# Kernel tuning notes

Measured on AMD Instinct MI355X. Metric: run time of the kernel, lower is better.

Reference implementation:

```python
import jax, jax.numpy as jnp
import numpy as np

NH, NKV, D = 16, 8, 128
HID = 2048
EPS = 1e-6
ROPE_BASE = 10000.0
T = 2048


def setup_inputs() -> dict:
    key = jax.random.key(0)
    k1, k2, k3 = jax.random.split(key, 3)
    return {
        "positions": jnp.arange(T, dtype=jnp.int32),
        "hidden_states": jax.random.normal(k1, (T, HID), dtype=jnp.float32),
        "w_qkv": jax.random.normal(k2, (HID, (NH + 2 * NKV) * D), dtype=jnp.float32) * 0.02,
        "w_o": jax.random.normal(k3, (NH * D, HID), dtype=jnp.float32) * 0.02,
        "q_norm_w": jnp.ones((D,), dtype=jnp.float32),
        "k_norm_w": jnp.ones((D,), dtype=jnp.float32),
    }


def _rmsnorm(x, w):
    # per-head RMSNorm over last dim (head_dim)
    return x * jax.lax.rsqrt(jnp.mean(x * x, axis=-1, keepdims=True) + EPS) * w


def reference(positions, hidden_states, w_qkv, w_o, q_norm_w, k_norm_w):
    t = hidden_states.shape[0]
    scale = D ** -0.5

    # fused QKV projection, then split
    qkv = hidden_states @ w_qkv                       # [T, (NH+2*NKV)*D]
    q, k, v = jnp.split(qkv, [NH * D, (NH + NKV) * D], axis=-1)
    q = q.reshape(t, NH, D)
    k = k.reshape(t, NKV, D)
    v = v.reshape(t, NKV, D)

    # per-head QK RMSNorm (Qwen3)
    q = _rmsnorm(q, q_norm_w)
    k = _rmsnorm(k, k_norm_w)

    # RoPE (neox style: rotate half-split pairs)
    inv_freq = 1.0 / (ROPE_BASE ** (jnp.arange(0, D, 2, dtype=jnp.float32) / D))
    freqs = positions.astype(jnp.float32)[:, None] * inv_freq  # [T, D/2]
    cos = jnp.cos(freqs)[:, None, :]                   # [T, 1, D/2]
    sin = jnp.sin(freqs)[:, None, :]

    def rope(x):
        x1, x2 = jnp.split(x, 2, axis=-1)
        return jnp.concatenate([x1 * cos - x2 * sin, x2 * cos + x1 * sin], axis=-1)

    q = rope(q)
    k = rope(k)

    # GQA: repeat kv heads
    g = NH // NKV
    kr = jnp.repeat(k, g, axis=1)                      # [T, NH, D]
    vr = jnp.repeat(v, g, axis=1)

    # causal attention
    scores = jnp.einsum('thd,shd->hts', q, kr) * scale  # [NH, T, T]
    causal = jnp.tril(jnp.ones((t, t), dtype=bool))
    scores = jnp.where(causal[None], scores, -jnp.inf)
    probs = jax.nn.softmax(scores, axis=-1)
    o = jnp.einsum('hts,shd->thd', probs, vr).reshape(t, NH * D)

    return o @ w_o
```

## Files before the change

### kernel.cpp

```cpp
#include <hip/hip_runtime.h>
#include <math.h>

#define T_TOK 2048
#define HIDDEN 2048
#define NH 16
#define NKV 8
#define DH 128

typedef unsigned short u16;
typedef __attribute__((ext_vector_type(8))) short bf16x8;
typedef __attribute__((ext_vector_type(4))) float f32x4;

__device__ __forceinline__ u16 f2bf(float f) {
  union { float f; unsigned u; } x; x.f = f;
  unsigned r = (x.u + 0x7fffu + ((x.u >> 16) & 1u)) >> 16;
  return (u16)r;
}

__device__ __forceinline__ float bf2f(u16 v) {
  union { unsigned u; float f; } x; x.u = ((unsigned)v) << 16;
  return x.f;
}

__device__ __forceinline__ void gload16(const void* g, void* l) {
  __builtin_amdgcn_global_load_lds((const __attribute__((address_space(1))) void*)g,
                                   (__attribute__((address_space(3))) void*)l,
                                   16, 0, 0);
}

__global__ __launch_bounds__(256) void prepass(const float* __restrict__ hidden,
                                               const float* __restrict__ w_qkv,
                                               const float* __restrict__ w_o,
                                               u16* __restrict__ Xb,
                                               u16* __restrict__ WqkvT,
                                               u16* __restrict__ WoT) {
  __shared__ float tile[64][65];
  const int b = blockIdx.x;
  if (b < 4096) {
    int i = b * 256 + threadIdx.x;
    float4 v = ((const float4*)hidden)[i];
    ushort4 o;
    o.x = f2bf(v.x); o.y = f2bf(v.y); o.z = f2bf(v.z); o.w = f2bf(v.w);
    ((ushort4*)Xb)[i] = o;
    return;
  }
  const float* in; u16* out; int R, Cdim, c0, r0;
  if (b < 6144) {
    int bb = b - 4096;
    in = w_qkv; out = WqkvT; R = 2048; Cdim = 4096;
    c0 = (bb & 63) * 64; r0 = (bb >> 6) * 64;
  } else {
    int bb = b - 6144;
    in = w_o; out = WoT; R = 2048; Cdim = 2048;
    c0 = (bb & 31) * 64; r0 = (bb >> 5) * 64;
  }
  const int tx = threadIdx.x & 63, ty = threadIdx.x >> 6;
#pragma unroll
  for (int i = 0; i < 64; i += 4)
    tile[ty + i][tx] = in[(size_t)(r0 + ty + i) * Cdim + c0 + tx];
  __syncthreads();
#pragma unroll
  for (int i = 0; i < 64; i += 4)
    out[(size_t)(c0 + ty + i) * R + r0 + tx] = f2bf(tile[tx][ty + i]);
}

__global__ __launch_bounds__(256) void add_parts4(const u16* __restrict__ a,
                                                  const u16* __restrict__ b,
                                                  const u16* __restrict__ c,
                                                  const u16* __restrict__ d,
                                                  float* __restrict__ o, int n4) {
  int i = blockIdx.x * blockDim.x + threadIdx.x;
  if (i < n4) {
    ushort4 x = ((const ushort4*)a)[i], y = ((const ushort4*)b)[i];
    ushort4 u = ((const ushort4*)c)[i], v = ((const ushort4*)d)[i];
    float4 z;
    z.x = bf2f(x.x) + bf2f(y.x) + bf2f(u.x) + bf2f(v.x);
    z.y = bf2f(x.y) + bf2f(y.y) + bf2f(u.y) + bf2f(v.y);
    z.z = bf2f(x.z) + bf2f(y.z) + bf2f(u.z) + bf2f(v.z);
    z.w = bf2f(x.w) + bf2f(y.w) + bf2f(u.w) + bf2f(v.w);
    ((float4*)o)[i] = z;
  }
}

__global__ __launch_bounds__(256) void rope_vt(const u16* __restrict__ qkv0,
                                               const u16* __restrict__ qkv1,
                                               const int* __restrict__ pos,
                                               const float* __restrict__ qw,
                                               const float* __restrict__ kw,
                                               u16* __restrict__ Qg,
                                               u16* __restrict__ Kg,
                                               u16* __restrict__ Vt,
                                               unsigned* __restrict__ counter) {
  __shared__ float tile[64][65];
  const int b = blockIdx.x;
  if (b < 12288) {
    const int wave = threadIdx.x >> 6, j = threadIdx.x & 63;
    const int idx = b * 4 + wave;
    const int t = idx & 2047, slot = idx >> 11;
    const float QSC = 0.088388347648318447f * 1.4426950408889634f;
    const size_t base_i = (size_t)t * 4096 + slot * 128;
    float x1 = bf2f(qkv0[base_i + j]) + bf2f(qkv1[base_i + j]);
    float x2 = bf2f(qkv0[base_i + j + 64]) + bf2f(qkv1[base_i + j + 64]);
    float ss = x1 * x1 + x2 * x2;
#pragma unroll
    for (int m = 1; m < 64; m <<= 1) ss += __shfl_xor(ss, m);
    float r = rsqrtf(ss * (1.0f / 128.0f) + 1e-6f);
    const bool isq = slot < NH;
    const float* w = isq ? qw : kw;
    float xn1 = x1 * r * w[j], xn2 = x2 * r * w[j + 64];
    float fp = (float)pos[t];
    float inv_freq = exp2f(-(float)j * (13.287712379549449f / 64.0f));
    float ang = fp * inv_freq;
    float sn, cs;
    sincosf(ang, &sn, &cs);
    float o1 = xn1 * cs - xn2 * sn;
    float o2 = xn2 * cs + xn1 * sn;
    if (isq) {
      size_t base = ((size_t)slot * T_TOK + t) * DH;
      Qg[base + j] = f2bf(o1 * QSC); Qg[base + 64 + j] = f2bf(o2 * QSC);
    } else {
      size_t base = ((size_t)(slot - NH) * T_TOK + t) * DH;
      Kg[base + j] = f2bf(o1); Kg[base + 64 + j] = f2bf(o2);
    }
    return;
  }
  if (b == 12288 && threadIdx.x == 0) *counter = 0u;
  const int bb = b - 12288;
  const int h = bb & 7, rest = bb >> 3;
  const int t0 = (rest & 31) * 64, d0 = (rest >> 5) * 64;
  const int tx = threadIdx.x & 63, ty = threadIdx.x >> 6;
#pragma unroll
  for (int i = 0; i < 64; i += 4) {
    size_t gi = (size_t)(t0 + ty + i) * 4096 + (NH + NKV) * DH + h * DH + d0 + tx;
    tile[ty + i][tx] = bf2f(qkv0[gi]) + bf2f(qkv1[gi]);
  }
  __syncthreads();
#pragma unroll
  for (int i = 0; i < 64; i += 4)
    Vt[((size_t)h * DH + d0 + ty + i) * T_TOK + t0 + tx] = f2bf(tile[tx][ty + i]);
}

__global__ __launch_bounds__(256) void gemm_bf16(const u16* __restrict__ A,
                                                 const u16* __restrict__ Bt,
                                                 void* __restrict__ Cout,
                                                 int M, int N, int K, int lda, int ldb,
                                                 int obf16) {
  __shared__ u16 Alds[128 * 64];
  __shared__ u16 Blds[128 * 64];
  A += (size_t)blockIdx.z * K;
  Bt += (size_t)blockIdx.z * K;
  const int m0 = blockIdx.y * 128, n0 = blockIdx.x * 128;
  const int wave = threadIdx.x >> 6, lane = threadIdx.x & 63;
  const int l15 = lane & 15, quad = lane >> 4;
  const int wr = wave >> 1, wc = wave & 1;

  const f32x4 zero = {0.f, 0.f, 0.f, 0.f};
  f32x4 acc[4][4];
#pragma unroll
  for (int i = 0; i < 4; ++i)
#pragma unroll
    for (int j = 0; j < 4; ++j) acc[i][j] = zero;

  for (int k0 = 0; k0 < K; k0 += 64) {
    __syncthreads();
#pragma unroll
    for (int c = 0; c < 4; ++c) {
      int chunk = wave * 4 + c;
      int slot = chunk * 64 + lane;
      int row = slot >> 3;
      int g = (slot & 7) ^ (row & 7);
      gload16(A + (size_t)(m0 + row) * lda + k0 + g * 8, &Alds[chunk * 512]);
      gload16(Bt + (size_t)(n0 + row) * ldb + k0 + g * 8, &Blds[chunk * 512]);
    }
    __syncthreads();
#pragma unroll
    for (int ksub = 0; ksub < 2; ++ksub) {
      bf16x8 af[4], bfr[4];
#pragma unroll
      for (int mt = 0; mt < 4; ++mt) {
        int r = wr * 64 + mt * 16 + l15;
        af[mt] = *(const bf16x8*)&Alds[r * 64 + (((ksub * 4 + quad) ^ (r & 7)) * 8)];
      }
#pragma unroll
      for (int nt = 0; nt < 4; ++nt) {
        int r = wc * 64 + nt * 16 + l15;
        bfr[nt] = *(const bf16x8*)&Blds[r * 64 + (((ksub * 4 + quad) ^ (r & 7)) * 8)];
      }
#pragma unroll
      for (int mt = 0; mt < 4; ++mt)
#pragma unroll
        for (int nt = 0; nt < 4; ++nt)
          acc[mt][nt] = __builtin_amdgcn_mfma_f32_16x16x32_bf16(af[mt], bfr[nt], acc[mt][nt], 0, 0, 0);
    }
  }
  if (obf16) {
    u16* C = (u16*)Cout + (size_t)blockIdx.z * M * N;
#pragma unroll
    for (int mt = 0; mt < 4; ++mt)
#pragma unroll
      for (int nt = 0; nt < 4; ++nt)
#pragma unroll
        for (int r = 0; r < 4; ++r)
          C[(size_t)(m0 + wr * 64 + mt * 16 + quad * 4 + r) * N + n0 + wc * 64 + nt * 16 + l15] =
              f2bf(acc[mt][nt][r]);
  } else {
    float* C = (float*)Cout + (size_t)blockIdx.z * M * N;
#pragma unroll
    for (int mt = 0; mt < 4; ++mt)
#pragma unroll
      for (int nt = 0; nt < 4; ++nt)
#pragma unroll
        for (int r = 0; r < 4; ++r)
          C[(size_t)(m0 + wr * 64 + mt * 16 + quad * 4 + r) * N + n0 + wc * 64 + nt * 16 + l15] =
              acc[mt][nt][r];
  }
}

__global__ __launch_bounds__(256) void attn_kernel(const u16* __restrict__ Qg,
                                                   const u16* __restrict__ Kg,
                                                   const u16* __restrict__ Vtg,
                                                   float* __restrict__ Opart,
                                                   float* __restrict__ Lpart,
                                                   unsigned* __restrict__ counter) {
  __shared__ u16 Klds[64 * 128];
  __shared__ u16 Vlds[128 * 64];
  __shared__ u16 Plds[4][16 * 72];
  __shared__ unsigned item_s;
  const int wave = threadIdx.x >> 6, lane = threadIdx.x & 63;
  const int l15 = lane & 15, quad = lane >> 4;
  u16* Pw = &Plds[wave][0];
  const f32x4 zero = {0.f, 0.f, 0.f, 0.f};
  const float4 zero4 = {0.f, 0.f, 0.f, 0.f};

  for (;;) {
    __syncthreads();
    if (threadIdx.x == 0) item_s = atomicAdd(counter, 1u);
    __syncthreads();
    const unsigned item = item_s;
    if (item >= 1024u) break;
    const int qt = 31 - (int)(item >> 5);
    const int s  = (int)(item >> 4) & 1;
    const int h  = (int)item & 15;
    const int kvh = h >> 1;
    const int slot = (h * 32 + qt) * 2 + s;
    const int j0 = s ? (qt + 2) >> 1 : 0;
    const int j1 = s ? qt + 1 : (qt + 2) >> 1;

    float* Oslot = Opart + (size_t)slot * (64 * 128);

    if (j0 >= j1) {
      for (int t = threadIdx.x; t < 64 * 128 / 4; t += 256) ((float4*)Oslot)[t] = zero4;
      if (threadIdx.x < 64) Lpart[slot * 64 + threadIdx.x] = 0.f;
      continue;
    }

    const u16* Qh = Qg + (size_t)h * T_TOK * DH;
    const u16* Kh = Kg + (size_t)kvh * T_TOK * DH;
    const u16* Vh = Vtg + (size_t)kvh * DH * T_TOK;
    const int qrow0 = qt * 64 + wave * 16;

    bf16x8 qf[4];
#pragma unroll
    for (int ks = 0; ks < 4; ++ks)
      qf[ks] = *(const bf16x8*)(Qh + (size_t)(qrow0 + l15) * DH + ks * 32 + quad * 8);

    f32x4 oacc[8];
#pragma unroll
    for (int i = 0; i < 8; ++i) oacc[i] = zero;
    float l_i[4] = {0.f, 0.f, 0.f, 0.f};

    for (int j = j0; j < j1; ++j) {
      __syncthreads();
#pragma unroll
      for (int c = 0; c < 4; ++c) {
        int chunk = wave * 4 + c;
        int sl = chunk * 64 + lane;
        {
          int ss = sl >> 4;
          int g = (sl & 15) ^ (ss & 15);
          gload16(Kh + ((size_t)(j * 64 + ss)) * DH + g * 8, &Klds[chunk * 512]);
        }
        {
          int d = sl >> 3;
          int g = (sl & 7) ^ (d & 7);
          gload16(Vh + (size_t)d * T_TOK + j * 64 + g * 8, &Vlds[chunk * 512]);
        }
      }
      __syncthreads();

      f32x4 sacc[4];
#pragma unroll
      for (int nt = 0; nt < 4; ++nt) sacc[nt] = zero;
#pragma unroll
      for (int nt = 0; nt < 4; ++nt) {
        int sr = nt * 16 + l15;
#pragma unroll
        for (int ks = 0; ks < 4; ++ks) {
          bf16x8 kf = *(const bf16x8*)&Klds[sr * 128 + (((ks * 4 + quad) ^ (sr & 15)) * 8)];
          sacc[nt] = __builtin_amdgcn_mfma_f32_16x16x32_bf16(qf[ks], kf, sacc[nt], 0, 0, 0);
        }
      }

      if (j == qt) {
#pragma unroll
        for (int nt = 0; nt < 4; ++nt)
#pragma unroll
          for (int r = 0; r < 4; ++r) {
            int col = j * 64 + nt * 16 + l15;
            int row = qrow0 + quad * 4 + r;
            if (col > row) sacc[nt][r] = -INFINITY;
          }
      }

#pragma unroll
      for (int nt = 0; nt < 4; ++nt)
#pragma unroll
        for (int r = 0; r < 4; ++r) {
          float pv = exp2f(sacc[nt][r]);
          unsigned u = __float_as_uint(pv);
          Pw[(quad * 4 + r) * 72 + nt * 16 + l15] = (u16)(u >> 16);
          l_i[r] += __uint_as_float(u & 0xffff0000u);
        }

      bf16x8 pf[2];
#pragma unroll
      for (int ks = 0; ks < 2; ++ks)
        pf[ks] = *(const bf16x8*)&Pw[l15 * 72 + ks * 32 + quad * 8];
#pragma unroll
      for (int ot = 0; ot < 8; ++ot) {
        int d = ot * 16 + l15;
#pragma unroll
        for (int ks = 0; ks < 2; ++ks) {
          bf16x8 vf = *(const bf16x8*)&Vlds[d * 64 + (((ks * 4 + quad) ^ (d & 7)) * 8)];
          oacc[ot] = __builtin_amdgcn_mfma_f32_16x16x32_bf16(pf[ks], vf, oacc[ot], 0, 0, 0);
        }
      }
    }

#pragma unroll
    for (int ot = 0; ot < 8; ++ot)
#pragma unroll
      for (int r = 0; r < 4; ++r)
        Oslot[(wave * 16 + quad * 4 + r) * 128 + ot * 16 + l15] = oacc[ot][r];
#pragma unroll
    for (int msk = 1; msk < 16; msk <<= 1)
#pragma unroll
      for (int r = 0; r < 4; ++r) l_i[r] += __shfl_xor(l_i[r], msk);
    if (l15 == 0) {
#pragma unroll
      for (int r = 0; r < 4; ++r)
        Lpart[slot * 64 + wave * 16 + quad * 4 + r] = l_i[r];
    }
  }
}

__global__ __launch_bounds__(256) void attn_merge(const float* __restrict__ Opart,
                                                  const float* __restrict__ Lpart,
                                                  u16* __restrict__ Og) {
  const int b = blockIdx.x;
  const int h = b & 15, qt = b >> 4;
  const int slot0 = (h * 32 + qt) * 2, slot1 = slot0 + 1;
  const float4* O0 = (const float4*)(Opart + (size_t)slot0 * (64 * 128));
  const float4* O1 = (const float4*)(Opart + (size_t)slot1 * (64 * 128));
#pragma unroll
  for (int it = 0; it < 8; ++it) {
    int idx = it * 256 + threadIdx.x;
    int r = idx >> 5, c4 = idx & 31;
    float rl = 1.0f / (Lpart[slot0 * 64 + r] + Lpart[slot1 * 64 + r]);
    float4 a = O0[idx], c = O1[idx];
    int row = qt * 64 + r, col = c4 * 4;
    u16* dst = Og + (size_t)row * (NH * DH) + h * DH + col;
    dst[0] = f2bf((a.x + c.x) * rl);
    dst[1] = f2bf((a.y + c.y) * rl);
    dst[2] = f2bf((a.z + c.z) * rl);
    dst[3] = f2bf((a.w + c.w) * rl);
  }
}

extern "C" void kernel_launch(void* const* d_in, const int* in_sizes, int n_in,
                              void* d_out, int out_size, void* d_ws, size_t ws_size,
                              hipStream_t stream) {
  (void)in_sizes; (void)n_in; (void)out_size; (void)ws_size;
  const int* positions = (const int*)d_in[0];
  const float* hidden  = (const float*)d_in[1];
  const float* w_qkv   = (const float*)d_in[2];
  const float* w_o     = (const float*)d_in[3];
  const float* q_norm  = (const float*)d_in[4];
  const float* k_norm  = (const float*)d_in[5];
  float* out = (float*)d_out;

  char* ws = (char*)d_ws;
  u16*   Xb    = (u16*)(ws);
  u16*   WqkvT = (u16*)(ws + ( 8ull << 20));
  u16*   WoT   = (u16*)(ws + (24ull << 20));
  u16*   P0    = (u16*)(ws + (32ull << 20));
  u16*   P1    = P0 + (size_t)T_TOK * 4096;
  u16*   Qg    = (u16*)(ws + (64ull << 20));
  u16*   Kg    = (u16*)(ws + (72ull << 20));
  u16*   Vt    = (u16*)(ws + (76ull << 20));
  u16*   AttnO = (u16*)(ws + (80ull << 20));
  float* Opart = (float*)(ws + (32ull << 20));
  float* Lpart = (float*)(ws);
  unsigned* ctr = (unsigned*)(ws + (512ull << 10));
  u16*   G2P   = (u16*)(ws + (32ull << 20));

  prepass<<<dim3(7168), 256, 0, stream>>>(hidden, w_qkv, w_o, Xb, WqkvT, WoT);

  gemm_bf16<<<dim3(4096 / 128, T_TOK / 128, 2), 256, 0, stream>>>(
      Xb, WqkvT, P0, T_TOK, 4096, 1024, HIDDEN, HIDDEN, 1);

  rope_vt<<<dim3(12288 + 512), 256, 0, stream>>>(P0, P1, positions,
                                                 q_norm, k_norm, Qg, Kg, Vt, ctr);

  attn_kernel<<<dim3(768), 256, 0, stream>>>(Qg, Kg, Vt, Opart, Lpart, ctr);
  attn_merge<<<dim3(512), 256, 0, stream>>>(Opart, Lpart, AttnO);

  gemm_bf16<<<dim3(HIDDEN / 128, T_TOK / 128, 4), 256, 0, stream>>>(
      AttnO, WoT, G2P, T_TOK, HIDDEN, 512, NH * DH, NH * DH, 1);
  const int n4 = T_TOK * HIDDEN / 4;
  add_parts4<<<dim3(n4 / 256), 256, 0, stream>>>(
      G2P, G2P + (size_t)T_TOK * HIDDEN, G2P + 2 * (size_t)T_TOK * HIDDEN,
      G2P + 3 * (size_t)T_TOK * HIDDEN, out, n4);
}
```

Measured before the change: 259.7 us.

## Fuse attention merge into attention kernel via completion flags; reduce split-K parts

Removes the separate attn_merge launch. The attention kernel now writes normalized bf16 output directly when a tile needs no split. For split tiles, the second finishing block (detected via a per-tile atomic flag after a threadfence) performs the merge. Empty split halves are now skipped instead of writing zeros. Also adds an XOR-swizzled P layout in LDS in place of the padded stride, raises the attention grid and occupancy hint, and halves the output projection's split-K factor so the final add reads two partial buffers instead of four. In exchange it depends on correct fence and flag ordering across blocks, and the output GEMM has fewer blocks to run in parallel.

```diff
diff --git a/kernel.cpp b/kernel.cpp
--- a/kernel.cpp
+++ b/kernel.cpp
@@ -64,20 +64,17 @@
     out[(size_t)(c0 + ty + i) * R + r0 + tx] = f2bf(tile[tx][ty + i]);
 }
 
-__global__ __launch_bounds__(256) void add_parts4(const u16* __restrict__ a,
+__global__ __launch_bounds__(256) void add_parts2(const u16* __restrict__ a,
                                                   const u16* __restrict__ b,
-                                                  const u16* __restrict__ c,
-                                                  const u16* __restrict__ d,
                                                   float* __restrict__ o, int n4) {
   int i = blockIdx.x * blockDim.x + threadIdx.x;
   if (i < n4) {
     ushort4 x = ((const ushort4*)a)[i], y = ((const ushort4*)b)[i];
-    ushort4 u = ((const ushort4*)c)[i], v = ((const ushort4*)d)[i];
     float4 z;
-    z.x = bf2f(x.x) + bf2f(y.x) + bf2f(u.x) + bf2f(v.x);
-    z.y = bf2f(x.y) + bf2f(y.y) + bf2f(u.y) + bf2f(v.y);
-    z.z = bf2f(x.z) + bf2f(y.z) + bf2f(u.z) + bf2f(v.z);
-    z.w = bf2f(x.w) + bf2f(y.w) + bf2f(u.w) + bf2f(v.w);
+    z.x = bf2f(x.x) + bf2f(y.x);
+    z.y = bf2f(x.y) + bf2f(y.y);
+    z.z = bf2f(x.z) + bf2f(y.z);
+    z.w = bf2f(x.w) + bf2f(y.w);
     ((float4*)o)[i] = z;
   }
 }
@@ -90,7 +87,8 @@
                                                u16* __restrict__ Qg,
                                                u16* __restrict__ Kg,
                                                u16* __restrict__ Vt,
-                                               unsigned* __restrict__ counter) {
+                                               unsigned* __restrict__ counter,
+                                               unsigned* __restrict__ flags) {
   __shared__ float tile[64][65];
   const int b = blockIdx.x;
   if (b < 12288) {
@@ -124,7 +122,11 @@
     }
     return;
   }
-  if (b == 12288 && threadIdx.x == 0) *counter = 0u;
+  if (b == 12288) {
+    if (threadIdx.x == 0) *counter = 0u;
+    flags[threadIdx.x] = 0u;
+    flags[threadIdx.x + 256] = 0u;
+  }
   const int bb = b - 12288;
   const int h = bb & 7, rest = bb >> 3;
   const int t0 = (rest & 31) * 64, d0 = (rest >> 5) * 64;
@@ -216,27 +218,28 @@
   }
 }
 
-__global__ __launch_bounds__(256) void attn_kernel(const u16* __restrict__ Qg,
-                                                   const u16* __restrict__ Kg,
-                                                   const u16* __restrict__ Vtg,
-                                                   float* __restrict__ Opart,
-                                                   float* __restrict__ Lpart,
-                                                   unsigned* __restrict__ counter) {
+__global__ __launch_bounds__(256, 4) void attn_kernel(const u16* __restrict__ Qg,
+                                                      const u16* __restrict__ Kg,
+                                                      const u16* __restrict__ Vtg,
+                                                      float* __restrict__ Opart,
+                                                      float* __restrict__ Lpart,
+                                                      unsigned* __restrict__ counter,
+                                                      unsigned* __restrict__ flags,
+                                                      u16* __restrict__ Og) {
   __shared__ u16 Klds[64 * 128];
   __shared__ u16 Vlds[128 * 64];
-  __shared__ u16 Plds[4][16 * 72];
-  __shared__ unsigned item_s;
+  __shared__ u16 Plds[4][16 * 64];
+  unsigned* shq = (unsigned*)&Plds[0][0];
   const int wave = threadIdx.x >> 6, lane = threadIdx.x & 63;
   const int l15 = lane & 15, quad = lane >> 4;
   u16* Pw = &Plds[wave][0];
   const f32x4 zero = {0.f, 0.f, 0.f, 0.f};
-  const float4 zero4 = {0.f, 0.f, 0.f, 0.f};
 
   for (;;) {
     __syncthreads();
-    if (threadIdx.x == 0) item_s = atomicAdd(counter, 1u);
-    __syncthreads();
-    const unsigned item = item_s;
+    if (threadIdx.x == 0) shq[0] = atomicAdd(counter, 1u);
+    __syncthreads();
+    const unsigned item = shq[0];
     if (item >= 1024u) break;
     const int qt = 31 - (int)(item >> 5);
     const int s  = (int)(item >> 4) & 1;
@@ -245,14 +248,7 @@
     const int slot = (h * 32 + qt) * 2 + s;
     const int j0 = s ? (qt + 2) >> 1 : 0;
     const int j1 = s ? qt + 1 : (qt + 2) >> 1;
-
-    float* Oslot = Opart + (size_t)slot * (64 * 128);
-
-    if (j0 >= j1) {
-      for (int t = threadIdx.x; t < 64 * 128 / 4; t += 256) ((float4*)Oslot)[t] = zero4;
-      if (threadIdx.x < 64) Lpart[slot * 64 + threadIdx.x] = 0.f;
-      continue;
-    }
+    if (j0 >= j1) continue;
 
     const u16* Qh = Qg + (size_t)h * T_TOK * DH;
     const u16* Kh = Kg + (size_t)kvh * T_TOK * DH;
@@ -318,14 +314,16 @@
         for (int r = 0; r < 4; ++r) {
           float pv = exp2f(sacc[nt][r]);
           unsigned u = __float_as_uint(pv);
-          Pw[(quad * 4 + r) * 72 + nt * 16 + l15] = (u16)(u >> 16);
+          int row = quad * 4 + r;
+          int c = nt * 16 + l15;
+          Pw[row * 64 + (((c >> 3) ^ (row & 7)) * 8) + (c & 7)] = (u16)(u >> 16);
           l_i[r] += __uint_as_float(u & 0xffff0000u);
         }
 
       bf16x8 pf[2];
 #pragma unroll
       for (int ks = 0; ks < 2; ++ks)
-        pf[ks] = *(const bf16x8*)&Pw[l15 * 72 + ks * 32 + quad * 8];
+        pf[ks] = *(const bf16x8*)&Pw[l15 * 64 + (((ks * 4 + quad) ^ (l15 & 7)) * 8)];
 #pragma unroll
       for (int ot = 0; ot < 8; ++ot) {
         int d = ot * 16 + l15;
@@ -338,42 +336,58 @@
     }
 
 #pragma unroll
+    for (int msk = 1; msk < 16; msk <<= 1)
+#pragma unroll
+      for (int r = 0; r < 4; ++r) l_i[r] += __shfl_xor(l_i[r], msk);
+
+    if (j0 == 0 && j1 == qt + 1) {
+      float rl[4];
+#pragma unroll
+      for (int r = 0; r < 4; ++r) rl[r] = 1.0f / l_i[r];
+#pragma unroll
+      for (int ot = 0; ot < 8; ++ot)
+#pragma unroll
+        for (int r = 0; r < 4; ++r) {
+          int row = qrow0 + quad * 4 + r;
+          Og[(size_t)row * (NH * DH) + h * DH + ot * 16 + l15] = f2bf(oacc[ot][r] * rl[r]);
+        }
+      continue;
+    }
+
+    float* Oslot = Opart + (size_t)slot * (64 * 128);
+#pragma unroll
     for (int ot = 0; ot < 8; ++ot)
 #pragma unroll
       for (int r = 0; r < 4; ++r)
         Oslot[(wave * 16 + quad * 4 + r) * 128 + ot * 16 + l15] = oacc[ot][r];
-#pragma unroll
-    for (int msk = 1; msk < 16; msk <<= 1)
-#pragma unroll
-      for (int r = 0; r < 4; ++r) l_i[r] += __shfl_xor(l_i[r], msk);
     if (l15 == 0) {
 #pragma unroll
       for (int r = 0; r < 4; ++r)
         Lpart[slot * 64 + wave * 16 + quad * 4 + r] = l_i[r];
     }
-  }
-}
-
-__global__ __launch_bounds__(256) void attn_merge(const float* __restrict__ Opart,
-                                                  const float* __restrict__ Lpart,
-                                                  u16* __restrict__ Og) {
-  const int b = blockIdx.x;
-  const int h = b & 15, qt = b >> 4;
-  const int slot0 = (h * 32 + qt) * 2, slot1 = slot0 + 1;
-  const float4* O0 = (const float4*)(Opart + (size_t)slot0 * (64 * 128));
-  const float4* O1 = (const float4*)(Opart + (size_t)slot1 * (64 * 128));
-#pragma unroll
-  for (int it = 0; it < 8; ++it) {
-    int idx = it * 256 + threadIdx.x;
-    int r = idx >> 5, c4 = idx & 31;
-    float rl = 1.0f / (Lpart[slot0 * 64 + r] + Lpart[slot1 * 64 + r]);
-    float4 a = O0[idx], c = O1[idx];
-    int row = qt * 64 + r, col = c4 * 4;
-    u16* dst = Og + (size_t)row * (NH * DH) + h * DH + col;
-    dst[0] = f2bf((a.x + c.x) * rl);
-    dst[1] = f2bf((a.y + c.y) * rl);
-    dst[2] = f2bf((a.z + c.z) * rl);
-    dst[3] = f2bf((a.w + c.w) * rl);
+    __threadfence();
+    __syncthreads();
+    if (threadIdx.x == 0) shq[1] = atomicAdd(&flags[h * 32 + qt], 1u);
+    __syncthreads();
+    if (shq[1] == 1u) {
+      __threadfence();
+      const int slot0 = (h * 32 + qt) * 2, slot1 = slot0 + 1;
+      const float4* O0 = (const float4*)(Opart + (size_t)slot0 * (64 * 128));
+      const float4* O1 = (const float4*)(Opart + (size_t)slot1 * (64 * 128));
+#pragma unroll
+      for (int it = 0; it < 8; ++it) {
+        int idx = it * 256 + threadIdx.x;
+        int r = idx >> 5, c4 = idx & 31;
+        float rl = 1.0f / (Lpart[slot0 * 64 + r] + Lpart[slot1 * 64 + r]);
+        float4 a = O0[idx], c = O1[idx];
+        int row = qt * 64 + r, col = c4 * 4;
+        u16* dst = Og + (size_t)row * (NH * DH) + h * DH + col;
+        dst[0] = f2bf((a.x + c.x) * rl);
+        dst[1] = f2bf((a.y + c.y) * rl);
+        dst[2] = f2bf((a.z + c.z) * rl);
+        dst[3] = f2bf((a.w + c.w) * rl);
+      }
+    }
   }
 }
 
@@ -401,7 +415,8 @@
   u16*   AttnO = (u16*)(ws + (80ull << 20));
   float* Opart = (float*)(ws + (32ull << 20));
   float* Lpart = (float*)(ws);
-  unsigned* ctr = (unsigned*)(ws + (512ull << 10));
+  unsigned* ctr   = (unsigned*)(ws + (512ull << 10));
+  unsigned* flags = (unsigned*)(ws + (1024ull << 10));
   u16*   G2P   = (u16*)(ws + (32ull << 20));
 
   prepass<<<dim3(7168), 256, 0, stream>>>(hidden, w_qkv, w_o, Xb, WqkvT, WoT);
@@ -410,15 +425,13 @@
       Xb, WqkvT, P0, T_TOK, 4096, 1024, HIDDEN, HIDDEN, 1);
 
   rope_vt<<<dim3(12288 + 512), 256, 0, stream>>>(P0, P1, positions,
-                                                 q_norm, k_norm, Qg, Kg, Vt, ctr);
-
-  attn_kernel<<<dim3(768), 256, 0, stream>>>(Qg, Kg, Vt, Opart, Lpart, ctr);
-  attn_merge<<<dim3(512), 256, 0, stream>>>(Opart, Lpart, AttnO);
-
-  gemm_bf16<<<dim3(HIDDEN / 128, T_TOK / 128, 4), 256, 0, stream>>>(
-      AttnO, WoT, G2P, T_TOK, HIDDEN, 512, NH * DH, NH * DH, 1);
+                                                 q_norm, k_norm, Qg, Kg, Vt, ctr, flags);
+
+  attn_kernel<<<dim3(1024), 256, 0, stream>>>(Qg, Kg, Vt, Opart, Lpart, ctr, flags, AttnO);
+
+  gemm_bf16<<<dim3(HIDDEN / 128, T_TOK / 128, 2), 256, 0, stream>>>(
+      AttnO, WoT, G2P, T_TOK, HIDDEN, 1024, NH * DH, NH * DH, 1);
   const int n4 = T_TOK * HIDDEN / 4;
-  add_parts4<<<dim3(n4 / 256), 256, 0, stream>>>(
-      G2P, G2P + (size_t)T_TOK * HIDDEN, G2P + 2 * (size_t)T_TOK * HIDDEN,
-      G2P + 3 * (size_t)T_TOK * HIDDEN, out, n4);
-}
+  add_parts2<<<dim3(n4 / 256), 256, 0, stream>>>(
+      G2P, G2P + (size_t)T_TOK * HIDDEN, out, n4);
+}
```

New measurement: 485.7 us. 1.87x slower.
